# Kernel optimization log

Measured on AMD Instinct MI355X. Metric: run time of the kernel, lower is better.

## Reference

```python
import jax, jax.numpy as jnp
import numpy as np

B, V, D, H, W = 2, 256, 512, 256, 256
CH = 96  # RED-CNN channels


def conv2d(x, w, b=None, padding='SAME'):
    y = jax.lax.conv_general_dilated(x, w, (1, 1), padding,
                                     dimension_numbers=('NCHW', 'OIHW', 'NCHW'))
    if b is not None:
        y = y + b[None, :, None, None]
    return y


def backproject_per_view(fp, angles):
    # fp: [B,V,D] filtered sinogram; one single-view backprojection per angle -> [B,V,H,W]
    b = fp.shape[0]
    ys = jnp.arange(H, dtype=jnp.float32) - (H - 1) / 2.
    xs = jnp.arange(W, dtype=jnp.float32) - (W - 1) / 2.
    Y, X = jnp.meshgrid(ys, xs, indexing='ij')
    c = jnp.cos(angles)[:, None, None]
    s = jnp.sin(angles)[:, None, None]
    u = X[None] * c + Y[None] * s + (D - 1) / 2.  # [V,H,W] detector coordinate
    u0 = jnp.floor(u)
    frac = (u - u0).reshape(1, V, H * W)
    u0i = u0.astype(jnp.int32)
    valid = ((u0i >= 0) & (u0i <= D - 2)).reshape(1, V, H * W)
    u0c = jnp.clip(u0i, 0, D - 2).reshape(V, H * W)
    idx0 = jnp.broadcast_to(u0c[None], (b, V, H * W))
    g0 = jnp.take_along_axis(fp, idx0, axis=2)
    g1 = jnp.take_along_axis(fp, idx0 + 1, axis=2)
    g = (g0 * (1. - frac) + g1 * frac) * valid
    return (g * (jnp.pi / V)).reshape(b, V, H, W)


def red_cnn(x, enc_w0, enc_w, enc_b, dec_w, dec_wN, dec_b, dec_bN):
    relu = jax.nn.relu
    r1 = x
    h = relu(conv2d(x, enc_w0, enc_b[0]))
    h = relu(conv2d(h, enc_w[0], enc_b[1])); r2 = h
    h = relu(conv2d(h, enc_w[1], enc_b[2]))
    h = relu(conv2d(h, enc_w[2], enc_b[3])); r3 = h
    h = relu(conv2d(h, enc_w[3], enc_b[4]))
    h = relu(conv2d(h, dec_w[0], dec_b[0]) + r3)
    h = relu(conv2d(h, dec_w[1], dec_b[1]))
    h = relu(conv2d(h, dec_w[2], dec_b[2]) + r2)
    h = relu(conv2d(h, dec_w[3], dec_b[3]))
    return relu(conv2d(h, dec_wN, dec_bN) + r1)


def setup_inputs():
    key = jax.random.key(0)
    ks = jax.random.split(key, 8)
    p = jax.random.normal(ks[0], (B, 1, V, D), dtype=jnp.float32)
    proj_weight = jax.random.uniform(ks[1], (1, 1, V, D), dtype=jnp.float32, minval=0.5, maxval=1.5)
    # Ram-Lak ramp filter, length 2*D-1 (matches padding=(0, num_det-1))
    n = np.arange(-(D - 1), D)
    h = np.zeros(2 * D - 1, dtype=np.float32)
    h[D - 1] = 0.25
    odd = (n % 2) != 0
    h[odd] = -1.0 / (np.pi * n[odd]) ** 2
    ramp = jnp.asarray(h).reshape(1, 1, 1, 2 * D - 1)
    views = jnp.arange(V, dtype=jnp.float32) * (2 * jnp.pi / V)
    std = 0.01
    conv_w = std * jax.random.normal(ks[2], (1, V, 3, 3), dtype=jnp.float32)
    conv_b = jnp.zeros((1,), jnp.float32)
    enc_w0 = std * jax.random.normal(ks[3], (CH, 1, 5, 5), dtype=jnp.float32)
    enc_w = std * jax.random.normal(ks[4], (4, CH, CH, 5, 5), dtype=jnp.float32)
    enc_b = jnp.zeros((5, CH), jnp.float32)
    dec_w = std * jax.random.normal(ks[5], (4, CH, CH, 5, 5), dtype=jnp.float32)
    dec_wN = std * jax.random.normal(ks[6], (1, CH, 5, 5), dtype=jnp.float32)
    dec_b = jnp.zeros((4, CH), jnp.float32)
    dec_bN = jnp.zeros((1,), jnp.float32)
    return dict(p=p, proj_weight=proj_weight, ramp=ramp, views=views,
                conv_w=conv_w, conv_b=conv_b, enc_w0=enc_w0, enc_w=enc_w,
                enc_b=enc_b, dec_w=dec_w, dec_wN=dec_wN, dec_b=dec_b, dec_bN=dec_bN)


def reference(p, proj_weight, ramp, views, conv_w, conv_b, enc_w0, enc_w,
              enc_b, dec_w, dec_wN, dec_b, dec_bN):
    p_w = p * proj_weight
    filtered = conv2d(p_w, ramp, padding=[(0, 0), (D - 1, D - 1)])  # [B,1,V,D]
    x = backproject_per_view(filtered[:, 0], views)                 # [B,V,H,W]
    x_sorted = jnp.sort(x, axis=1)                                  # cross-view sort
    x_in = conv2d(x_sorted, conv_w, conv_b)                         # [B,1,H,W]
    return red_cnn(x_in, enc_w0, enc_w, enc_b, dec_w, dec_wN, dec_b, dec_bN)
```

## Files before the change

kernel.cpp:

```cpp
#include <hip/hip_runtime.h>
#include <hip/hip_fp16.h>
#include <math.h>

#define B_ 2
#define V_ 256
#define D_ 512
#define H_ 256
#define W_ 256
#define CH_ 96

typedef _Float16 f16;
typedef f16 half8 __attribute__((ext_vector_type(8)));
typedef f16 half4 __attribute__((ext_vector_type(4)));
typedef f16 half2v __attribute__((ext_vector_type(2)));
typedef float f32x16 __attribute__((ext_vector_type(16)));

#if defined(__has_builtin)
#if __has_builtin(__builtin_amdgcn_fdot2)
#define FDOT2(a, b, c) __builtin_amdgcn_fdot2((a), (b), (c), false)
#endif
#endif
#ifndef FDOT2
#define FDOT2(a, b, c) ((c) + (float)(a)[0] * (float)(b)[0] + (float)(a)[1] * (float)(b)[1])
#endif

__global__ void filter_kernel(const float* __restrict__ p,
                              const float* __restrict__ pw,
                              const float* __restrict__ ramp,
                              float* __restrict__ filt) {
  int v = blockIdx.x, b = blockIdx.y, t = threadIdx.x;
  __shared__ float s_pw[D_];
  __shared__ float s_ramp[2 * D_ - 1];
  const float* prow = p + (size_t)(b * V_ + v) * D_;
  const float* wrow = pw + (size_t)v * D_;
  s_pw[t] = prow[t] * wrow[t];
  s_pw[t + 256] = prow[t + 256] * wrow[t + 256];
  for (int i = t; i < 2 * D_ - 1; i += 256) s_ramp[i] = ramp[i];
  __syncthreads();
  float acc0 = 0.f, acc1 = 0.f;
  for (int m = 0; m < D_; ++m) {
    float x = s_pw[m];
    acc0 += x * s_ramp[m - t + (D_ - 1)];
    acc1 += x * s_ramp[m - (t + 256) + (D_ - 1)];
  }
  filt[(size_t)(b * V_ + v) * D_ + t] = acc0;
  filt[(size_t)(b * V_ + v) * D_ + t + 256] = acc1;
}

__global__ __launch_bounds__(256) void backproj_sort_kernel(
    const float* __restrict__ filt,
    const float* __restrict__ views,
    f16* __restrict__ xt) {
  __shared__ float s_c[V_], s_s[V_];
  int tid = threadIdx.x;
  int b = blockIdx.y;
  {
    float sn, cs;
    sincosf(views[tid], &sn, &cs);
    s_c[tid] = cs;
    s_s[tid] = sn;
  }
  __syncthreads();
  int lane = tid & 63;
  int wv = tid >> 6;
  int pix = blockIdx.x * 4 + wv;
  int h = pix >> 8, w = pix & 255;
  float X = (float)w - (W_ - 1) * 0.5f;
  float Y = (float)h - (H_ - 1) * 0.5f;
  const float* filt_b = filt + (size_t)b * V_ * D_;
  float r[4];
  #pragma unroll
  for (int i = 0; i < 4; ++i) {
    int v = lane * 4 + i;
    float u = X * s_c[v] + Y * s_s[v] + (D_ - 1) * 0.5f;
    float u0 = floorf(u);
    float frac = u - u0;
    int u0i = (int)u0;
    bool valid = (u0i >= 0) && (u0i <= D_ - 2);
    int u0c = min(max(u0i, 0), D_ - 2);
    const float* frow = filt_b + (size_t)v * D_;
    float g0 = frow[u0c], g1 = frow[u0c + 1];
    r[i] = valid ? (g0 * (1.f - frac) + g1 * frac) * (float)(M_PI / V_) : 0.f;
  }
  half2v A = { (f16)r[0], (f16)r[1] };
  half2v B = { (f16)r[2], (f16)r[3] };
  #pragma unroll
  for (int k = 2; k <= 256; k <<= 1) {
    #pragma unroll
    for (int j = k >> 1; j > 0; j >>= 1) {
      if (j >= 4) {
        int jl = j >> 2;
        bool low = (lane & jl) == 0;
        bool up = (lane & (k >> 2)) == 0;
        bool keepmin = (low == up);
        int ia = __builtin_bit_cast(int, A);
        int ib = __builtin_bit_cast(int, B);
        half2v Ao = __builtin_bit_cast(half2v, __shfl_xor(ia, jl, 64));
        half2v Bo = __builtin_bit_cast(half2v, __shfl_xor(ib, jl, 64));
        half2v Amn = __builtin_elementwise_min(A, Ao);
        half2v Amx = __builtin_elementwise_max(A, Ao);
        half2v Bmn = __builtin_elementwise_min(B, Bo);
        half2v Bmx = __builtin_elementwise_max(B, Bo);
        A = keepmin ? Amn : Amx;
        B = keepmin ? Bmn : Bmx;
      } else if (j == 2) {
        bool up = (lane & (k >> 2)) == 0;
        half2v mn = __builtin_elementwise_min(A, B);
        half2v mx = __builtin_elementwise_max(A, B);
        A = up ? mn : mx;
        B = up ? mx : mn;
      } else {
        unsigned ua = __builtin_bit_cast(unsigned, A);
        unsigned ub = __builtin_bit_cast(unsigned, B);
        half2v As = __builtin_bit_cast(half2v, (ua >> 16) | (ua << 16));
        half2v Bs = __builtin_bit_cast(half2v, (ub >> 16) | (ub << 16));
        unsigned amn = __builtin_bit_cast(unsigned, __builtin_elementwise_min(A, As));
        unsigned amx = __builtin_bit_cast(unsigned, __builtin_elementwise_max(A, As));
        unsigned bmn = __builtin_bit_cast(unsigned, __builtin_elementwise_min(B, Bs));
        unsigned bmx = __builtin_bit_cast(unsigned, __builtin_elementwise_max(B, Bs));
        unsigned Aasc  = (amn & 0xFFFFu) | (amx & 0xFFFF0000u);
        unsigned Adesc = (amx & 0xFFFFu) | (amn & 0xFFFF0000u);
        unsigned Basc  = (bmn & 0xFFFFu) | (bmx & 0xFFFF0000u);
        unsigned Bdesc = (bmx & 0xFFFFu) | (bmn & 0xFFFF0000u);
        bool upA, upB;
        if (k == 2) { upA = true; upB = false; }
        else { upA = upB = ((lane & (k >> 2)) == 0); }
        A = __builtin_bit_cast(half2v, upA ? Aasc : Adesc);
        B = __builtin_bit_cast(half2v, upB ? Basc : Bdesc);
      }
    }
  }
  half4 o;
  o[0] = A[0]; o[1] = A[1]; o[2] = B[0]; o[3] = B[1];
  *(half4*)(xt + ((size_t)b * (H_ * W_) + pix) * V_ + lane * 4) = o;
}

__global__ __launch_bounds__(256) void conv_vred_kernel(
    const f16* __restrict__ xt,
    const float* __restrict__ cw,
    const float* __restrict__ cb,
    float* __restrict__ xin) {
  int tid = threadIdx.x;
  int b = blockIdx.y;
  int lane = tid & 63, wv = tid >> 6;
  int pix = blockIdx.x * 4 + wv;
  int h = pix >> 8, w = pix & 255;
  const f16* xtb = xt + (size_t)b * (H_ * W_) * V_;
  float wr[9][4];
  #pragma unroll
  for (int tap = 0; tap < 9; ++tap)
    #pragma unroll
    for (int i = 0; i < 4; ++i)
      wr[tap][i] = cw[(lane * 4 + i) * 9 + tap];
  float acc = 0.f;
  #pragma unroll
  for (int dy = -1; dy <= 1; ++dy) {
    int hh = h + dy;
    if (hh < 0 || hh >= H_) continue;
    #pragma unroll
    for (int dx = -1; dx <= 1; ++dx) {
      int ww = w + dx;
      if (ww < 0 || ww >= W_) continue;
      const f16* base = xtb + (((size_t)hh << 8) + ww) * V_ + lane * 4;
      half4 x4 = *(const half4*)base;
      int tap = (dy + 1) * 3 + dx + 1;
      acc += (float)x4[0] * wr[tap][0] + (float)x4[1] * wr[tap][1] +
             (float)x4[2] * wr[tap][2] + (float)x4[3] * wr[tap][3];
    }
  }
  for (int off = 32; off > 0; off >>= 1) acc += __shfl_down(acc, off);
  if (lane == 0) xin[(size_t)b * (H_ * W_) + pix] = acc + cb[0];
}

__global__ void wtrans_kernel(const float* __restrict__ enc_w,
                              const float* __restrict__ dec_w,
                              f16* __restrict__ wT) {
  int idx = blockIdx.x * 256 + threadIdx.x;
  const int TOT = 8 * 25 * 96 * 96;
  if (idx >= TOT) return;
  int ci16 = idx & 15;
  int t1 = idx >> 4;
  int co = t1 % 96;
  int t2 = t1 / 96;
  int cig = t2 % 6;
  int t3 = t2 / 6;
  int tap = t3 % 25;
  int l = t3 / 25;
  int ci = cig * 16 + ci16;
  const float* src = (l < 4) ? (enc_w + (size_t)l * 96 * 96 * 25)
                             : (dec_w + (size_t)(l - 4) * 96 * 96 * 25);
  wT[idx] = (f16)src[((size_t)co * 96 + ci) * 25 + tap];
}

__global__ __launch_bounds__(768, 3) void conv5_mfma_kernel(
    const f16* __restrict__ act,
    const f16* __restrict__ wTl,
    const float* __restrict__ bias,
    const f16* __restrict__ res,
    f16* __restrict__ outp) {
  int tid = threadIdx.x;
  int lane = tid & 63;
  int l31 = lane & 31, lh = lane >> 5;
  int wvi = tid >> 6;
  int c = wvi >> 2;
  int q = wvi & 3;
  int bt = blockIdx.x;
  int x0 = (bt & 7) * 32;
  int y0 = (bt >> 3) * 16;
  size_t bofs = (size_t)blockIdx.z * ((size_t)H_ * W_ * CH_);
  const f16* actb = act + bofs;

  __shared__ __align__(16) f16 tile[6 * 20 * 36 * 16];
  char* tb = (char*)tile;
  const int PLANE = 20 * 36 * 32;
  const int ROWB  = 36 * 32;

  {
    int cell = tid;
    if (cell < 720) {
      int row = cell / 36, xx = cell % 36;
      int gy = y0 + row - 2, gx = x0 + xx - 2;
      bool va = (gy >= 0 && gy < H_ && gx >= 0 && gx < W_);
      int swz = ((xx >> 2) & 7) << 4;
      int b0 = cell * 32;
      int d0 = b0 ^ swz, d1 = (b0 + 16) ^ swz;
      const uint4 z4 = {0u, 0u, 0u, 0u};
      const uint4* sp = (const uint4*)(actb + ((size_t)(gy * W_ + gx)) * CH_);
      #pragma unroll
      for (int g = 0; g < 6; ++g) {
        uint4 v0 = z4, v1 = z4;
        if (va) { v0 = sp[2 * g]; v1 = sp[2 * g + 1]; }
        *(uint4*)(tb + g * PLANE + d0) = v0;
        *(uint4*)(tb + g * PLANE + d1) = v1;
      }
    }
  }
  __syncthreads();

  int dsb[5];
  #pragma unroll
  for (int dx = 0; dx < 5; ++dx) {
    int xr = l31 + dx;
    dsb[dx] = (xr * 32 + lh * 16) ^ (((xr >> 2) & 7) << 4);
  }

  f32x16 acc[4];
  #pragma unroll
  for (int i = 0; i < 4; ++i)
    #pragma unroll
    for (int r = 0; r < 16; ++r) acc[i][r] = 0.f;

  const f16* wc = wTl + (size_t)(c * 32 + l31) * 16 + lh * 8;

  for (int cig = 0; cig < 6; ++cig) {
    const f16* wcg = wc + (size_t)cig * (96 * 16);
    char* pb = tb + cig * PLANE + 4 * q * ROWB;
    #pragma unroll
    for (int dx = 0; dx < 5; ++dx) {
      half8 Af[5];
      #pragma unroll
      for (int dy = 0; dy < 5; ++dy)
        Af[dy] = *(const half8*)(wcg + (size_t)(dy * 5 + dx) * (6 * 96 * 16));
      half8 Bw[8];
      #pragma unroll
      for (int k = 0; k < 8; ++k)
        Bw[k] = *(const half8*)(pb + k * ROWB + dsb[dx]);
      #pragma unroll
      for (int dy = 0; dy < 5; ++dy) {
        acc[0] = __builtin_amdgcn_mfma_f32_32x32x16_f16(Af[dy], Bw[dy + 0], acc[0], 0, 0, 0);
        acc[1] = __builtin_amdgcn_mfma_f32_32x32x16_f16(Af[dy], Bw[dy + 1], acc[1], 0, 0, 0);
        acc[2] = __builtin_amdgcn_mfma_f32_32x32x16_f16(Af[dy], Bw[dy + 2], acc[2], 0, 0, 0);
        acc[3] = __builtin_amdgcn_mfma_f32_32x32x16_f16(Af[dy], Bw[dy + 3], acc[3], 0, 0, 0);
      }
    }
  }

  int x = x0 + l31;
  #pragma unroll
  for (int i = 0; i < 4; ++i) {
    int y = y0 + 4 * q + i;
    f32x16 a = acc[i];
    size_t po = bofs + ((size_t)(y * W_ + x)) * CH_ + c * 32;
    #pragma unroll
    for (int g = 0; g < 4; ++g) {
      int cob = g * 8 + lh * 4;
      half4 rv;
      if (res) rv = *(const half4*)(res + po + cob);
      half4 o4;
      #pragma unroll
      for (int r = 0; r < 4; ++r) {
        float v = a[g * 4 + r] + bias[c * 32 + cob + r];
        if (res) v += (float)rv[r];
        o4[r] = (f16)fmaxf(v, 0.f);
      }
      *(half4*)(outp + po + cob) = o4;
    }
  }
}

__global__ __launch_bounds__(256) void conv5_first_kernel(
    const float* __restrict__ xin, const float* __restrict__ w0,
    const float* __restrict__ bias, f16* __restrict__ A) {
  int tid = threadIdx.x;
  int x0 = (blockIdx.x & 15) * 16, y0 = (blockIdx.x >> 4) * 16;
  const float* xb = xin + (size_t)blockIdx.y * (H_ * W_);
  __shared__ float t[20][20];
  __shared__ float ws[CH_ * 25];
  for (int i = tid; i < 400; i += 256) {
    int r = i / 20, cc = i % 20;
    int gy = y0 + r - 2, gx = x0 + cc - 2;
    t[r][cc] = (gy >= 0 && gy < H_ && gx >= 0 && gx < W_) ? xb[gy * W_ + gx] : 0.f;
  }
  for (int i = tid; i < CH_ * 25; i += 256) ws[i] = w0[i];
  __syncthreads();
  int pg = tid >> 3;
  int ch0 = (tid & 7) * 12;
  float acc8[8][12];
  #pragma unroll
  for (int j = 0; j < 8; ++j)
    #pragma unroll
    for (int cc = 0; cc < 12; ++cc) acc8[j][cc] = bias[ch0 + cc];
  #pragma unroll
  for (int k = 0; k < 25; ++k) {
    int ky = k / 5, kx = k % 5;
    float xv8[8];
    #pragma unroll
    for (int j = 0; j < 8; ++j) {
      int px = pg * 8 + j;
      int ty = px >> 4, tx = px & 15;
      xv8[j] = t[ty + ky][tx + kx];
    }
    #pragma unroll
    for (int cc = 0; cc < 12; ++cc) {
      float wv = ws[(ch0 + cc) * 25 + k];
      #pragma unroll
      for (int j = 0; j < 8; ++j) acc8[j][cc] = fmaf(xv8[j], wv, acc8[j][cc]);
    }
  }
  size_t base = (size_t)blockIdx.y * (H_ * W_);
  #pragma unroll
  for (int j = 0; j < 8; ++j) {
    int px = pg * 8 + j;
    int ty = px >> 4, tx = px & 15;
    f16* Ap = A + (base + (size_t)((y0 + ty) * W_ + x0 + tx)) * CH_ + ch0;
    f16 tmp[12];
    #pragma unroll
    for (int cc = 0; cc < 12; ++cc) tmp[cc] = (f16)fmaxf(acc8[j][cc], 0.f);
    #pragma unroll
    for (int u = 0; u < 3; ++u)
      *(uint2*)(Ap + u * 4) = *(uint2*)(tmp + u * 4);
  }
}

__global__ __launch_bounds__(256) void conv5_last_kernel(
    const f16* __restrict__ A, const float* __restrict__ wN,
    const float* __restrict__ bias, const float* __restrict__ xin,
    float* __restrict__ outp) {
  int tid = threadIdx.x;
  int tx = tid & 15, ty = tid >> 4;
  int x0 = (blockIdx.x & 15) * 16, y0 = (blockIdx.x >> 4) * 16;
  size_t bo = (size_t)blockIdx.y * (H_ * W_);
  const f16* Ab = A + bo * CH_;
  __shared__ __align__(16) f16 t[400 * CH_];
  __shared__ __align__(16) f16 wh[25 * CH_];
  char* tb = (char*)t;
  for (int i = tid; i < 25 * CH_; i += 256) {
    int k = i / CH_, ci = i % CH_;
    wh[i] = (f16)wN[ci * 25 + k];
  }
  for (int cell = tid; cell < 400; cell += 256) {
    int r = cell / 20, cc = cell % 20;
    int gy = y0 + r - 2, gx = x0 + cc - 2;
    bool va = (gy >= 0 && gy < H_ && gx >= 0 && gx < W_);
    const uint4 z4 = {0u, 0u, 0u, 0u};
    const uint4* sp = (const uint4*)(Ab + ((size_t)(gy * W_ + gx)) * CH_);
    int cb = cell * 192;
    int sw = (cell & 7) << 4;
    #pragma unroll
    for (int j = 0; j < 12; ++j) {
      uint4 v = va ? sp[j] : z4;
      *(uint4*)(tb + ((cb + j * 16) ^ sw)) = v;
    }
  }
  __syncthreads();
  float acc = bias[0];
  #pragma unroll
  for (int k = 0; k < 25; ++k) {
    int cellr = (ty + k / 5) * 20 + tx + k % 5;
    int cb = cellr * 192;
    int sw = (cellr & 7) << 4;
    const half2v* wp = (const half2v*)(wh + k * CH_);
    #pragma unroll
    for (int c2 = 0; c2 < 12; ++c2) {
      uint4 av = *(const uint4*)(tb + ((cb + c2 * 16) ^ sw));
      acc = FDOT2(__builtin_bit_cast(half2v, av.x), wp[c2 * 4 + 0], acc);
      acc = FDOT2(__builtin_bit_cast(half2v, av.y), wp[c2 * 4 + 1], acc);
      acc = FDOT2(__builtin_bit_cast(half2v, av.z), wp[c2 * 4 + 2], acc);
      acc = FDOT2(__builtin_bit_cast(half2v, av.w), wp[c2 * 4 + 3], acc);
    }
  }
  int pix = (y0 + ty) * W_ + x0 + tx;
  acc += xin[bo + pix];
  outp[bo + pix] = fmaxf(acc, 0.f);
}

__global__ void diag_kernel(float* __restrict__ out, int code, int wsMiB) {
  out[0] = (float)(code * 1000000 + wsMiB);
}

extern "C" void kernel_launch(void* const* d_in, const int* in_sizes, int n_in,
                              void* d_out, int out_size, void* d_ws, size_t ws_size,
                              hipStream_t stream) {
  const float* p       = (const float*)d_in[0];
  const float* pweight = (const float*)d_in[1];
  const float* ramp    = (const float*)d_in[2];
  const float* views   = (const float*)d_in[3];
  const float* conv_w  = (const float*)d_in[4];
  const float* conv_b  = (const float*)d_in[5];
  const float* enc_w0  = (const float*)d_in[6];
  const float* enc_w   = (const float*)d_in[7];
  const float* enc_b   = (const float*)d_in[8];
  const float* dec_w   = (const float*)d_in[9];
  const float* dec_wN  = (const float*)d_in[10];
  const float* dec_b   = (const float*)d_in[11];
  const float* dec_bN  = (const float*)d_in[12];
  float* out           = (float*)d_out;

  char* wsb   = (char*)d_ws;
  float* filt = (float*)(wsb);
  float* xin  = (float*)(wsb + 0x100000u);
  f16* wT     = (f16*)(wsb + 0x180000u);
  const size_t AOFF = 0x508000u;
  f16* xt     = (f16*)(wsb + AOFF);

  const size_t ACT = (size_t)H_ * W_ * CH_;
  const size_t NEEDED_SEQ  = AOFF + 3 * ACT * 2;
  const size_t NEEDED_DUAL = AOFF + 6 * ACT * 2;
  int wsMiB = (int)(ws_size >> 20);
  if (ws_size < NEEDED_SEQ) {
    diag_kernel<<<1, 1, 0, stream>>>(out, 9, wsMiB);
    return;
  }
  int nb = (ws_size >= NEEDED_DUAL) ? 2 : 1;
  size_t bufSz = (size_t)nb * ACT;
  f16* A  = (f16*)(wsb + AOFF);
  f16* Bb = A + bufSz;
  f16* C  = Bb + bufSz;

  const int HW = H_ * W_;
  const size_t WTL = 25 * 96 * 96;

  filter_kernel<<<dim3(V_, B_), 256, 0, stream>>>(p, pweight, ramp, filt);
  wtrans_kernel<<<7200, 256, 0, stream>>>(enc_w, dec_w, wT);

  if (nb == 2) {
    backproj_sort_kernel<<<dim3(HW / 4, 2), 256, 0, stream>>>(filt, views, xt);
    conv_vred_kernel<<<dim3(HW / 4, 2), 256, 0, stream>>>(xt, conv_w, conv_b, xin);
  } else {
    for (int b = 0; b < B_; ++b) {
      backproj_sort_kernel<<<dim3(HW / 4, 1), 256, 0, stream>>>(filt + (size_t)b * V_ * D_, views, xt);
      conv_vred_kernel<<<dim3(HW / 4, 1), 256, 0, stream>>>(xt, conv_w, conv_b, xin + (size_t)b * HW);
    }
  }

  auto run_net = [&](const float* xin_g, float* out_g, int nbat) {
    dim3 gL(128, 1, nbat);
    dim3 gS(256, nbat);
    conv5_first_kernel<<<gS, 256, 0, stream>>>(xin_g, enc_w0, enc_b, A);
    conv5_mfma_kernel<<<gL, 768, 0, stream>>>(A,  wT + 0 * WTL, enc_b + 96,  nullptr, Bb);
    conv5_mfma_kernel<<<gL, 768, 0, stream>>>(Bb, wT + 1 * WTL, enc_b + 192, nullptr, A);
    conv5_mfma_kernel<<<gL, 768, 0, stream>>>(A,  wT + 2 * WTL, enc_b + 288, nullptr, C);
    conv5_mfma_kernel<<<gL, 768, 0, stream>>>(C,  wT + 3 * WTL, enc_b + 384, nullptr, A);
    conv5_mfma_kernel<<<gL, 768, 0, stream>>>(A,  wT + 4 * WTL, dec_b + 0,   C,       C);
    conv5_mfma_kernel<<<gL, 768, 0, stream>>>(C,  wT + 5 * WTL, dec_b + 96,  nullptr, A);
    conv5_mfma_kernel<<<gL, 768, 0, stream>>>(A,  wT + 6 * WTL, dec_b + 192, Bb,      Bb);
    conv5_mfma_kernel<<<gL, 768, 0, stream>>>(Bb, wT + 7 * WTL, dec_b + 288, nullptr, A);
    conv5_last_kernel<<<gS, 256, 0, stream>>>(A, dec_wN, dec_bN, xin_g, out_g);
  };

  if (nb == 2) {
    run_net(xin, out, 2);
  } else {
    for (int b = 0; b < B_; ++b)
      run_net(xin + (size_t)b * HW, out + (size_t)b * HW, 1);
  }
}
```

Baseline: 668.6 us.

## Switch activation layout to channel-group planes of 16 channels

Changes the activation tensor layout from pixel-major NHWC with 96 channels to six planes of 16 channels each. The conv tile loads, residual reads and output stores are rewritten to match, and so are the first and last conv kernels. The first conv kernel is also restructured so each thread handles one pixel across all channels. Each tile load now reads contiguous 32-byte chunks within a plane, which is meant to improve coalescing. In exchange it adds more address arithmetic, and the first conv now does its 25-tap loop per channel with weight reads from shared memory.

```diff
diff --git a/kernel.cpp b/kernel.cpp
--- a/kernel.cpp
+++ b/kernel.cpp
@@ -23,6 +23,7 @@
 #ifndef FDOT2
 #define FDOT2(a, b, c) ((c) + (float)(a)[0] * (float)(b)[0] + (float)(a)[1] * (float)(b)[1])
 #endif
+
 
 __global__ void filter_kernel(const float* __restrict__ p,
                               const float* __restrict__ pw,
@@ -214,24 +215,23 @@
   char* tb = (char*)tile;
   const int PLANE = 20 * 36 * 32;
   const int ROWB  = 36 * 32;
-
-  {
-    int cell = tid;
-    if (cell < 720) {
-      int row = cell / 36, xx = cell % 36;
-      int gy = y0 + row - 2, gx = x0 + xx - 2;
-      bool va = (gy >= 0 && gy < H_ && gx >= 0 && gx < W_);
-      int swz = ((xx >> 2) & 7) << 4;
-      int b0 = cell * 32;
-      int d0 = b0 ^ swz, d1 = (b0 + 16) ^ swz;
-      const uint4 z4 = {0u, 0u, 0u, 0u};
-      const uint4* sp = (const uint4*)(actb + ((size_t)(gy * W_ + gx)) * CH_);
-      #pragma unroll
-      for (int g = 0; g < 6; ++g) {
-        uint4 v0 = z4, v1 = z4;
-        if (va) { v0 = sp[2 * g]; v1 = sp[2 * g + 1]; }
-        *(uint4*)(tb + g * PLANE + d0) = v0;
-        *(uint4*)(tb + g * PLANE + d1) = v1;
+  const size_t GSTR = (size_t)H_ * W_ * 16;
+
+  #pragma unroll
+  for (int g = 0; g < 6; ++g) {
+    const f16* gb = actb + (size_t)g * GSTR;
+    #pragma unroll
+    for (int pass = 0; pass < 2; ++pass) {
+      int idx = pass * 768 + tid;
+      int cell = idx >> 1, j = idx & 1;
+      if (cell < 720) {
+        int row = cell / 36, xx = cell % 36;
+        int gy = y0 + row - 2, gx = x0 + xx - 2;
+        bool va = (gy >= 0 && gy < H_ && gx >= 0 && gx < W_);
+        uint4 v = {0u, 0u, 0u, 0u};
+        if (va) v = *(const uint4*)(gb + ((size_t)(gy * W_ + gx)) * 16 + j * 8);
+        int swz = ((xx >> 2) & 7) << 4;
+        *(uint4*)(tb + g * PLANE + ((cell * 32 + j * 16) ^ swz)) = v;
       }
     }
   }
@@ -279,21 +279,22 @@
   #pragma unroll
   for (int i = 0; i < 4; ++i) {
     int y = y0 + 4 * q + i;
+    int p = y * W_ + x;
     f32x16 a = acc[i];
-    size_t po = bofs + ((size_t)(y * W_ + x)) * CH_ + c * 32;
     #pragma unroll
     for (int g = 0; g < 4; ++g) {
-      int cob = g * 8 + lh * 4;
+      int cg = c * 2 + (g >> 1);
+      size_t ao = bofs + (size_t)cg * GSTR + (size_t)p * 16 + (g & 1) * 8 + lh * 4;
       half4 rv;
-      if (res) rv = *(const half4*)(res + po + cob);
+      if (res) rv = *(const half4*)(res + ao);
       half4 o4;
       #pragma unroll
       for (int r = 0; r < 4; ++r) {
-        float v = a[g * 4 + r] + bias[c * 32 + cob + r];
+        float v = a[g * 4 + r] + bias[c * 32 + g * 8 + lh * 4 + r];
         if (res) v += (float)rv[r];
         o4[r] = (f16)fmaxf(v, 0.f);
       }
-      *(half4*)(outp + po + cob) = o4;
+      *(half4*)(outp + ao) = o4;
     }
   }
 }
@@ -302,6 +303,7 @@
     const float* __restrict__ xin, const float* __restrict__ w0,
     const float* __restrict__ bias, f16* __restrict__ A) {
   int tid = threadIdx.x;
+  int tx = tid & 15, ty = tid >> 4;
   int x0 = (blockIdx.x & 15) * 16, y0 = (blockIdx.x >> 4) * 16;
   const float* xb = xin + (size_t)blockIdx.y * (H_ * W_);
   __shared__ float t[20][20];
@@ -313,42 +315,26 @@
   }
   for (int i = tid; i < CH_ * 25; i += 256) ws[i] = w0[i];
   __syncthreads();
-  int pg = tid >> 3;
-  int ch0 = (tid & 7) * 12;
-  float acc8[8][12];
-  #pragma unroll
-  for (int j = 0; j < 8; ++j)
-    #pragma unroll
-    for (int cc = 0; cc < 12; ++cc) acc8[j][cc] = bias[ch0 + cc];
-  #pragma unroll
-  for (int k = 0; k < 25; ++k) {
-    int ky = k / 5, kx = k % 5;
-    float xv8[8];
-    #pragma unroll
-    for (int j = 0; j < 8; ++j) {
-      int px = pg * 8 + j;
-      int ty = px >> 4, tx = px & 15;
-      xv8[j] = t[ty + ky][tx + kx];
-    }
-    #pragma unroll
-    for (int cc = 0; cc < 12; ++cc) {
-      float wv = ws[(ch0 + cc) * 25 + k];
+  float xv[25];
+  #pragma unroll
+  for (int k = 0; k < 25; ++k) xv[k] = t[ty + k / 5][tx + k % 5];
+  size_t base = (size_t)blockIdx.y * ((size_t)H_ * W_ * CH_);
+  const size_t GSTR = (size_t)H_ * W_ * 16;
+  int p = (y0 + ty) * W_ + x0 + tx;
+  #pragma unroll
+  for (int g = 0; g < 6; ++g) {
+    f16 tmp[16];
+    #pragma unroll
+    for (int cc = 0; cc < 16; ++cc) {
+      int ch = g * 16 + cc;
+      float a0 = bias[ch];
       #pragma unroll
-      for (int j = 0; j < 8; ++j) acc8[j][cc] = fmaf(xv8[j], wv, acc8[j][cc]);
-    }
-  }
-  size_t base = (size_t)blockIdx.y * (H_ * W_);
-  #pragma unroll
-  for (int j = 0; j < 8; ++j) {
-    int px = pg * 8 + j;
-    int ty = px >> 4, tx = px & 15;
-    f16* Ap = A + (base + (size_t)((y0 + ty) * W_ + x0 + tx)) * CH_ + ch0;
-    f16 tmp[12];
-    #pragma unroll
-    for (int cc = 0; cc < 12; ++cc) tmp[cc] = (f16)fmaxf(acc8[j][cc], 0.f);
-    #pragma unroll
-    for (int u = 0; u < 3; ++u)
-      *(uint2*)(Ap + u * 4) = *(uint2*)(tmp + u * 4);
+      for (int k = 0; k < 25; ++k) a0 = fmaf(xv[k], ws[ch * 25 + k], a0);
+      tmp[cc] = (f16)fmaxf(a0, 0.f);
+    }
+    f16* Ap = A + base + g * GSTR + (size_t)p * 16;
+    *(uint4*)(Ap) = *(uint4*)(tmp);
+    *(uint4*)(Ap + 8) = *(uint4*)(tmp + 8);
   }
 }
 
@@ -361,25 +347,27 @@
   int x0 = (blockIdx.x & 15) * 16, y0 = (blockIdx.x >> 4) * 16;
   size_t bo = (size_t)blockIdx.y * (H_ * W_);
   const f16* Ab = A + bo * CH_;
-  __shared__ __align__(16) f16 t[400 * CH_];
+  const size_t GSTR = (size_t)H_ * W_ * 16;
+  __shared__ __align__(16) f16 t[6 * 400 * 16];
   __shared__ __align__(16) f16 wh[25 * CH_];
   char* tb = (char*)t;
+  const int LPLANE = 400 * 32;
   for (int i = tid; i < 25 * CH_; i += 256) {
     int k = i / CH_, ci = i % CH_;
     wh[i] = (f16)wN[ci * 25 + k];
   }
-  for (int cell = tid; cell < 400; cell += 256) {
-    int r = cell / 20, cc = cell % 20;
-    int gy = y0 + r - 2, gx = x0 + cc - 2;
-    bool va = (gy >= 0 && gy < H_ && gx >= 0 && gx < W_);
-    const uint4 z4 = {0u, 0u, 0u, 0u};
-    const uint4* sp = (const uint4*)(Ab + ((size_t)(gy * W_ + gx)) * CH_);
-    int cb = cell * 192;
-    int sw = (cell & 7) << 4;
-    #pragma unroll
-    for (int j = 0; j < 12; ++j) {
-      uint4 v = va ? sp[j] : z4;
-      *(uint4*)(tb + ((cb + j * 16) ^ sw)) = v;
+  #pragma unroll
+  for (int g = 0; g < 6; ++g) {
+    const f16* Ag = Ab + (size_t)g * GSTR;
+    for (int idx = tid; idx < 800; idx += 256) {
+      int cell = idx >> 1, j = idx & 1;
+      int r = cell / 20, cc = cell % 20;
+      int gy = y0 + r - 2, gx = x0 + cc - 2;
+      bool va = (gy >= 0 && gy < H_ && gx >= 0 && gx < W_);
+      uint4 v = {0u, 0u, 0u, 0u};
+      if (va) v = *(const uint4*)(Ag + ((size_t)(gy * W_ + gx)) * 16 + j * 8);
+      int sw = (cell & 7) << 4;
+      *(uint4*)(tb + g * LPLANE + ((cell * 32 + j * 16) ^ sw)) = v;
     }
   }
   __syncthreads();
@@ -387,16 +375,20 @@
   #pragma unroll
   for (int k = 0; k < 25; ++k) {
     int cellr = (ty + k / 5) * 20 + tx + k % 5;
-    int cb = cellr * 192;
     int sw = (cellr & 7) << 4;
-    const half2v* wp = (const half2v*)(wh + k * CH_);
-    #pragma unroll
-    for (int c2 = 0; c2 < 12; ++c2) {
-      uint4 av = *(const uint4*)(tb + ((cb + c2 * 16) ^ sw));
-      acc = FDOT2(__builtin_bit_cast(half2v, av.x), wp[c2 * 4 + 0], acc);
-      acc = FDOT2(__builtin_bit_cast(half2v, av.y), wp[c2 * 4 + 1], acc);
-      acc = FDOT2(__builtin_bit_cast(half2v, av.z), wp[c2 * 4 + 2], acc);
-      acc = FDOT2(__builtin_bit_cast(half2v, av.w), wp[c2 * 4 + 3], acc);
+    #pragma unroll
+    for (int g = 0; g < 6; ++g) {
+      const half2v* wp = (const half2v*)(wh + k * CH_ + g * 16);
+      uint4 a0 = *(const uint4*)(tb + g * LPLANE + ((cellr * 32) ^ sw));
+      uint4 a1 = *(const uint4*)(tb + g * LPLANE + ((cellr * 32 + 16) ^ sw));
+      acc = FDOT2(__builtin_bit_cast(half2v, a0.x), wp[0], acc);
+      acc = FDOT2(__builtin_bit_cast(half2v, a0.y), wp[1], acc);
+      acc = FDOT2(__builtin_bit_cast(half2v, a0.z), wp[2], acc);
+      acc = FDOT2(__builtin_bit_cast(half2v, a0.w), wp[3], acc);
+      acc = FDOT2(__builtin_bit_cast(half2v, a1.x), wp[4], acc);
+      acc = FDOT2(__builtin_bit_cast(half2v, a1.y), wp[5], acc);
+      acc = FDOT2(__builtin_bit_cast(half2v, a1.z), wp[6], acc);
+      acc = FDOT2(__builtin_bit_cast(half2v, a1.w), wp[7], acc);
     }
   }
   int pix = (y0 + ty) * W_ + x0 + tx;
```

New measurement: 663.1 us. About the same (-0.8%).
